# Performance work log

Measured on AMD Instinct MI355X. Metric: run time of the kernel, lower is better.

## Reference

```python
import jax, jax.numpy as jnp
import numpy as np

NB, NR = 100000, 200000            # bridge / road node counts
E_BR, E_RB, E_BB = 1000000, 1000000, 500000  # edges per relation
H = 32                             # hidden_channels


def _sage(h_src, h_dst, src, dst, n_dst, Wl, bl, Wr):
    # PyG SAGEConv: lin_l(mean_{j in N(i)} x_j) + lin_r(x_i); lin_r has no bias
    msg = jnp.take(h_src, src, axis=0)                      # [E, H] gather
    s = jax.ops.segment_sum(msg, dst, num_segments=n_dst)   # [n_dst, H] scatter-add
    cnt = jax.ops.segment_sum(jnp.ones((dst.shape[0],), h_src.dtype), dst, num_segments=n_dst)
    mean = s / jnp.maximum(cnt, 1.0)[:, None]                # mean aggregation
    return mean @ Wl + bl + h_dst @ Wr


def setup_inputs():
    key = jax.random.key(0)
    ks = jax.random.split(key, 24)
    n = lambda i, shape, s=0.1: jax.random.normal(ks[i], shape, jnp.float32) * s
    return {
        "x_bridge": n(0, (NB, 16), 1.0),
        "x_road": n(1, (NR, 8), 1.0),
        "src_br": jax.random.randint(ks[2], (E_BR,), 0, NB),
        "dst_br": jax.random.randint(ks[3], (E_BR,), 0, NR),
        "src_rb": jax.random.randint(ks[4], (E_RB,), 0, NR),
        "dst_rb": jax.random.randint(ks[5], (E_RB,), 0, NB),
        "src_bb": jax.random.randint(ks[6], (E_BB,), 0, NB),
        "dst_bb": jax.random.randint(ks[7], (E_BB,), 0, NB),
        "W_enc_b": n(8, (16, H)), "b_enc_b": n(9, (H,)),
        "W_enc_r": n(10, (8, H)), "b_enc_r": n(11, (H,)),
        "Wl_br": n(12, (H, H)), "bl_br": n(13, (H,)), "Wr_br": n(14, (H, H)),
        "Wl_rb": n(15, (H, H)), "bl_rb": n(16, (H,)), "Wr_rb": n(17, (H, H)),
        "Wl_bb": n(18, (H, H)), "bl_bb": n(19, (H,)), "Wr_bb": n(20, (H, H)),
        "Wo": n(21, (H, 1)), "bo": n(22, (1,)),
    }


def reference(x_bridge, x_road, src_br, dst_br, src_rb, dst_rb, src_bb, dst_bb,
              W_enc_b, b_enc_b, W_enc_r, b_enc_r,
              Wl_br, bl_br, Wr_br, Wl_rb, bl_rb, Wr_rb, Wl_bb, bl_bb, Wr_bb,
              Wo, bo):
    # per-node-type encoder + relu
    h_b = jax.nn.relu(x_bridge @ W_enc_b + b_enc_b)          # [NB, H]
    h_r = jax.nn.relu(x_road @ W_enc_r + b_enc_r)            # [NR, H]
    # HeteroConv(aggr='sum'): 'bridge' receives road->bridge and bridge->bridge.
    # (bridge->road output is dead code w.r.t. the returned bridge head; XLA DCEs it.)
    out_b = (_sage(h_r, h_b, src_rb, dst_rb, NB, Wl_rb, bl_rb, Wr_rb)
             + _sage(h_b, h_b, src_bb, dst_bb, NB, Wl_bb, bl_bb, Wr_bb))
    # relu then output Linear on 'bridge'
    return jax.nn.relu(out_b) @ Wo + bo                       # [NB, 1]
```

## Files before the change

### kernel.cpp

```cpp
#include <hip/hip_runtime.h>
#include <hip/hip_fp16.h>

#define H 32
#define TPB 256
#define EPT 16
#define SLOTS 128
#define CAP 2048
#define SUPB 2048
#define CAP1 22528
#define K2 4
#define NSUPMAX 128

__global__ void __launch_bounds__(TPB) prep_kernel(
        const float* __restrict__ x_b, const float* __restrict__ x_r,
        const float* __restrict__ W_b, const float* __restrict__ b_b,
        const float* __restrict__ W_r, const float* __restrict__ b_r,
        __half* __restrict__ h_b16, __half* __restrict__ h_r16,
        int NB, int NR, int encBlocks,
        const int* __restrict__ src_rb, const int* __restrict__ dst_rb,
        const int* __restrict__ src_bb, const int* __restrict__ dst_bb,
        int* __restrict__ gcur1, int* __restrict__ bins1,
        int E_RB, int E_BB, int NSUP) {
    int t = threadIdx.x;

    if (blockIdx.x < encBlocks) {
        __shared__ float sWb[16][H];
        __shared__ float sWr8[8][H];
        __shared__ float sbb[H];
        __shared__ float sbr[H];
        for (int i = t; i < 16 * H; i += TPB) ((float*)sWb)[i] = W_b[i];
        for (int i = t; i < 8 * H; i += TPB) ((float*)sWr8)[i] = W_r[i];
        if (t < H) { sbb[t] = b_b[t]; sbr[t] = b_r[t]; }
        __syncthreads();

        long long node = (long long)blockIdx.x * TPB + t;
        if (node < NB) {
            const float4* px = (const float4*)(x_b + node * 16);
            float acc[H];
            #pragma unroll
            for (int j = 0; j < H; ++j) acc[j] = sbb[j];
            #pragma unroll
            for (int c = 0; c < 4; ++c) {
                float4 q = px[c];
                float xs[4] = {q.x, q.y, q.z, q.w};
                #pragma unroll
                for (int u = 0; u < 4; ++u) {
                    int k = c * 4 + u;
                    #pragma unroll
                    for (int j = 0; j < H; ++j)
                        acc[j] = fmaf(xs[u], sWb[k][j], acc[j]);
                }
            }
            __half2 o[H / 2];
            #pragma unroll
            for (int j2 = 0; j2 < H / 2; ++j2)
                o[j2] = __floats2half2_rn(fmaxf(acc[2 * j2], 0.0f), fmaxf(acc[2 * j2 + 1], 0.0f));
            float4* dst = (float4*)(h_b16 + node * H);
            const float4* src = (const float4*)o;
            dst[0] = src[0]; dst[1] = src[1]; dst[2] = src[2]; dst[3] = src[3];
        } else if (node < (long long)NB + NR) {
            long long m = node - NB;
            const float4* px = (const float4*)(x_r + m * 8);
            float acc[H];
            #pragma unroll
            for (int j = 0; j < H; ++j) acc[j] = sbr[j];
            #pragma unroll
            for (int c = 0; c < 2; ++c) {
                float4 q = px[c];
                float xs[4] = {q.x, q.y, q.z, q.w};
                #pragma unroll
                for (int u = 0; u < 4; ++u) {
                    int k = c * 4 + u;
                    #pragma unroll
                    for (int j = 0; j < H; ++j)
                        acc[j] = fmaf(xs[u], sWr8[k][j], acc[j]);
                }
            }
            __half2 o[H / 2];
            #pragma unroll
            for (int j2 = 0; j2 < H / 2; ++j2)
                o[j2] = __floats2half2_rn(fmaxf(acc[2 * j2], 0.0f), fmaxf(acc[2 * j2 + 1], 0.0f));
            float4* dst = (float4*)(h_r16 + m * H);
            const float4* src = (const float4*)o;
            dst[0] = src[0]; dst[1] = src[1]; dst[2] = src[2]; dst[3] = src[3];
        }
    } else {
        __shared__ int lcnt[NSUPMAX];
        __shared__ int wbase[NSUPMAX];
        if (t < NSUPMAX) { lcnt[t] = 0; }
        __syncthreads();

        long long e0 = (long long)(blockIdx.x - encBlocks) * (TPB * EPT);
        long long EA = (long long)E_RB + E_BB;
        long long rb4 = (long long)(E_RB >> 2);
        int meta[EPT];

        #pragma unroll
        for (int j = 0; j < EPT / 4; ++j) {
            long long i4 = (e0 >> 2) + (long long)j * TPB + t;
            long long eb = i4 << 2;
            int dd[4];
            if (eb + 3 < (long long)E_RB) {
                int4 dv = ((const int4*)dst_rb)[i4];
                dd[0] = dv.x; dd[1] = dv.y; dd[2] = dv.z; dd[3] = dv.w;
            } else if (eb >= (long long)E_RB && eb + 3 < EA) {
                int4 dv = ((const int4*)dst_bb)[i4 - rb4];
                dd[0] = dv.x + NB; dd[1] = dv.y + NB; dd[2] = dv.z + NB; dd[3] = dv.w + NB;
            } else {
                #pragma unroll
                for (int u = 0; u < 4; ++u) {
                    long long e = eb + u;
                    dd[u] = (e < E_RB) ? dst_rb[e] : (e < EA ? NB + dst_bb[e - E_RB] : -1);
                }
            }
            #pragma unroll
            for (int u = 0; u < 4; ++u) {
                if (dd[u] >= 0) {
                    int sup = dd[u] >> 11;
                    int loc = atomicAdd(&lcnt[sup], 1);
                    meta[j * 4 + u] = (sup << 23) | (loc << 11) | (dd[u] & 2047);
                } else meta[j * 4 + u] = -1;
            }
        }
        __syncthreads();

        if (t < NSUP) {
            int c = lcnt[t];
            wbase[t] = c ? (t * CAP1 + atomicAdd(&gcur1[t * 16], c)) : 0;
        }
        __syncthreads();

        #pragma unroll
        for (int j = 0; j < EPT / 4; ++j) {
            long long i4 = (e0 >> 2) + (long long)j * TPB + t;
            long long eb = i4 << 2;
            int ss[4];
            if (eb + 3 < (long long)E_RB) {
                int4 sv = ((const int4*)src_rb)[i4];
                ss[0] = sv.x; ss[1] = sv.y; ss[2] = sv.z; ss[3] = sv.w;
            } else if (eb >= (long long)E_RB && eb + 3 < EA) {
                int4 sv = ((const int4*)src_bb)[i4 - rb4];
                ss[0] = sv.x; ss[1] = sv.y; ss[2] = sv.z; ss[3] = sv.w;
            } else {
                #pragma unroll
                for (int u = 0; u < 4; ++u) {
                    long long e = eb + u;
                    ss[u] = (e < E_RB) ? src_rb[e] : (e < EA ? (int)src_bb[e - E_RB] : 0);
                }
            }
            #pragma unroll
            for (int u = 0; u < 4; ++u) {
                int m = meta[j * 4 + u];
                if (m >= 0) {
                    int sup = (unsigned)m >> 23;
                    int loc = (m >> 11) & 0xFFF;
                    int gslot = wbase[sup] + loc;
                    if (gslot < (sup + 1) * CAP1)
                        bins1[gslot] = (ss[u] << 11) | (m & 2047);
                }
            }
        }
    }
}

__global__ void __launch_bounds__(TPB) placeB_kernel(
        const int* __restrict__ bins1, const int* __restrict__ gcur1,
        int* __restrict__ gcur2, int* __restrict__ bins, int NBUCK) {
    __shared__ int lcnt[16];
    __shared__ int wbase[16];
    __shared__ int lcur[16];
    int t = threadIdx.x;
    int sup = blockIdx.x / K2;
    int j   = blockIdx.x % K2;
    int n = gcur1[sup * 16];
    if (n > CAP1) n = CAP1;
    int chunk = (n + K2 - 1) / K2;
    int lo = j * chunk;
    int hi = lo + chunk; if (hi > n) hi = n;

    if (t < 16) lcnt[t] = 0;
    __syncthreads();

    const int* __restrict__ seg = bins1 + (long long)sup * CAP1;
    for (int i = lo + t; i < hi; i += TPB)
        atomicAdd(&lcnt[(seg[i] >> 7) & 15], 1);
    __syncthreads();

    if (t < 16) {
        int c = lcnt[t];
        int fb = sup * 16 + t;
        wbase[t] = (c && fb < NBUCK) ? (fb * CAP + atomicAdd(&gcur2[fb * 16], c)) : 0;
        lcur[t] = 0;
    }
    __syncthreads();

    for (int i = lo + t; i < hi; i += TPB) {
        int p = seg[i];
        int f = (p >> 7) & 15;
        int loc = atomicAdd(&lcur[f], 1);
        int fb = sup * 16 + f;
        int gslot = wbase[f] + loc;
        if (gslot < (fb + 1) * CAP)
            bins[gslot] = ((p >> 11) << 7) | (p & 127);
    }
}

__global__ void __launch_bounds__(TPB) buildgather_kernel(
        const __half* __restrict__ h_r16, const __half* __restrict__ h_b16,
        const int* __restrict__ bins, const int* __restrict__ gcur2,
        __half* __restrict__ mean16, int NB, int N2) {
    __shared__ int rawbuf[CAP];
    __shared__ int srcbuf[CAP];
    __shared__ int lcnt[SLOTS];
    __shared__ int lbase[SLOTS];
    __shared__ int lcur[SLOTS];
    __shared__ int tmp[SLOTS];
    int t = threadIdx.x;
    int b = blockIdx.x;
    int start = b * CAP;
    int n = gcur2[b * 16];
    if (n > CAP) n = CAP;

    if (t < SLOTS) lcnt[t] = 0;
    __syncthreads();

    {
        int n4 = n >> 2;
        const int4* bins4 = (const int4*)(bins + start);
        for (int i = t; i < n4; i += TPB) {
            int4 p = bins4[i];
            ((int4*)rawbuf)[i] = p;
            atomicAdd(&lcnt[p.x & 127], 1);
            atomicAdd(&lcnt[p.y & 127], 1);
            atomicAdd(&lcnt[p.z & 127], 1);
            atomicAdd(&lcnt[p.w & 127], 1);
        }
        for (int i = (n4 << 2) + t; i < n; i += TPB) {
            int packed = bins[start + i];
            rawbuf[i] = packed;
            atomicAdd(&lcnt[packed & 127], 1);
        }
    }
    __syncthreads();

    if (t < SLOTS) tmp[t] = lcnt[t];
    __syncthreads();
    for (int off = 1; off < SLOTS; off <<= 1) {
        int x = (t >= off && t < SLOTS) ? tmp[t - off] : 0;
        __syncthreads();
        if (t < SLOTS) tmp[t] += x;
        __syncthreads();
    }
    if (t < SLOTS) { lbase[t] = tmp[t] - lcnt[t]; lcur[t] = tmp[t] - lcnt[t]; }
    __syncthreads();

    for (int i = t; i < n; i += TPB) {
        int packed = rawbuf[i];
        int slot = atomicAdd(&lcur[packed & 127], 1);
        srcbuf[slot] = packed >> 7;
    }
    __syncthreads();

    int lane = t & 15, g = t >> 4;
    long long base_slot = (long long)b << 7;
    for (int sl = g; sl < SLOTS; sl += (TPB / 16)) {
        long long gd = base_slot + sl;
        if (gd >= N2) break;
        const __half* __restrict__ hs = (gd < NB) ? h_r16 : h_b16;
        int off = lbase[sl];
        int cnt = lcnt[sl];
        float ax = 0.0f, ay = 0.0f;
        int k = 0;
        for (; k + 8 <= cnt; k += 8) {
            int s[8];
            #pragma unroll
            for (int jj = 0; jj < 8; ++jj) s[jj] = srcbuf[off + k + jj];
            float2 f[8];
            #pragma unroll
            for (int jj = 0; jj < 8; ++jj)
                f[jj] = __half22float2(*(const __half2*)(hs + (long long)s[jj] * H + 2 * lane));
            #pragma unroll
            for (int jj = 0; jj < 8; ++jj) { ax += f[jj].x; ay += f[jj].y; }
        }
        if (k + 4 <= cnt) {
            int s[4];
            #pragma unroll
            for (int jj = 0; jj < 4; ++jj) s[jj] = srcbuf[off + k + jj];
            float2 f[4];
            #pragma unroll
            for (int jj = 0; jj < 4; ++jj)
                f[jj] = __half22float2(*(const __half2*)(hs + (long long)s[jj] * H + 2 * lane));
            #pragma unroll
            for (int jj = 0; jj < 4; ++jj) { ax += f[jj].x; ay += f[jj].y; }
            k += 4;
        }
        for (; k < cnt; ++k) {
            int s = srcbuf[off + k];
            float2 f = __half22float2(*(const __half2*)(hs + (long long)s * H + 2 * lane));
            ax += f.x; ay += f.y;
        }
        float inv = 1.0f / fmaxf((float)cnt, 1.0f);
        *(__half2*)(mean16 + gd * H + 2 * lane) = __floats2half2_rn(ax * inv, ay * inv);
    }
}

__global__ void __launch_bounds__(TPB) head_kernel(
        const __half* __restrict__ h_b16,
        const __half* __restrict__ mean16,
        const float* __restrict__ Wl_rb,
        const float* __restrict__ bl_rb,
        const float* __restrict__ Wl_bb,
        const float* __restrict__ bl_bb,
        const float* __restrict__ Wr_rb,
        const float* __restrict__ Wr_bb,
        const float* __restrict__ Wo,
        const float* __restrict__ bo,
        float* __restrict__ y, int N) {
    __shared__ float sWl_rb[H][H];
    __shared__ float sWl_bb[H][H];
    __shared__ float sWr[H][H];
    __shared__ float sbl[H];
    __shared__ float sWo[H];
    __shared__ float sbo;

    int t = threadIdx.x;
    for (int i = t; i < H * H; i += blockDim.x) {
        ((float*)sWl_rb)[i] = Wl_rb[i];
        ((float*)sWl_bb)[i] = Wl_bb[i];
        ((float*)sWr)[i]    = Wr_rb[i] + Wr_bb[i];
    }
    if (t < H) {
        sbl[t] = bl_rb[t] + bl_bb[t];
        sWo[t] = Wo[t];
    }
    if (t == 0) sbo = bo[0];
    __syncthreads();

    int node = blockIdx.x * TPB + t;
    if (node >= N) return;

    const float4* pr = (const float4*)(mean16 + (long long)node * H);
    const float4* pb = (const float4*)(mean16 + ((long long)N + node) * H);
    const float4* ph = (const float4*)(h_b16 + (long long)node * H);

    float acc[H];
    #pragma unroll
    for (int j = 0; j < H; ++j) acc[j] = sbl[j];

    #pragma unroll
    for (int c = 0; c < 4; ++c) {
        float4 qr = pr[c];
        float4 qb = pb[c];
        float4 qh = ph[c];
        const __half2* hr = (const __half2*)&qr;
        const __half2* hb = (const __half2*)&qb;
        const __half2* hh = (const __half2*)&qh;
        #pragma unroll
        for (int u = 0; u < 4; ++u) {
            float2 fr = __half22float2(hr[u]);
            float2 fb = __half22float2(hb[u]);
            float2 fh = __half22float2(hh[u]);
            int k0 = c * 8 + u * 2;
            #pragma unroll
            for (int j = 0; j < H; ++j) {
                acc[j] = fmaf(fr.x, sWl_rb[k0][j], acc[j]);
                acc[j] = fmaf(fb.x, sWl_bb[k0][j], acc[j]);
                acc[j] = fmaf(fh.x, sWr[k0][j], acc[j]);
                acc[j] = fmaf(fr.y, sWl_rb[k0 + 1][j], acc[j]);
                acc[j] = fmaf(fb.y, sWl_bb[k0 + 1][j], acc[j]);
                acc[j] = fmaf(fh.y, sWr[k0 + 1][j], acc[j]);
            }
        }
    }

    float out = 0.0f;
    #pragma unroll
    for (int j = 0; j < H; ++j)
        out = fmaf(fmaxf(acc[j], 0.0f), sWo[j], out);
    y[node] = out + sbo;
}

extern "C" void kernel_launch(void* const* d_in, const int* in_sizes, int n_in,
                              void* d_out, int out_size, void* d_ws, size_t ws_size,
                              hipStream_t stream) {
    const float* x_bridge = (const float*)d_in[0];
    const float* x_road   = (const float*)d_in[1];
    const int* src_rb = (const int*)d_in[4];
    const int* dst_rb = (const int*)d_in[5];
    const int* src_bb = (const int*)d_in[6];
    const int* dst_bb = (const int*)d_in[7];
    const float* W_enc_b = (const float*)d_in[8];
    const float* b_enc_b = (const float*)d_in[9];
    const float* W_enc_r = (const float*)d_in[10];
    const float* b_enc_r = (const float*)d_in[11];
    const float* Wl_rb = (const float*)d_in[15];
    const float* bl_rb = (const float*)d_in[16];
    const float* Wr_rb = (const float*)d_in[17];
    const float* Wl_bb = (const float*)d_in[18];
    const float* bl_bb = (const float*)d_in[19];
    const float* Wr_bb = (const float*)d_in[20];
    const float* Wo = (const float*)d_in[21];
    const float* bo = (const float*)d_in[22];
    float* y = (float*)d_out;

    const int NB = in_sizes[0] / 16;
    const int NR = in_sizes[1] / 8;
    const int E_RB = in_sizes[4];
    const int E_BB = in_sizes[6];
    const int N2 = 2 * NB;
    const long long E_ALL = (long long)E_RB + E_BB;
    const int NBUCK = (N2 + SLOTS - 1) / SLOTS;
    const int NSUP  = (N2 + SUPB - 1) / SUPB;

    char* wp = (char*)d_ws;
    __half* h_r16  = (__half*)wp; wp += (size_t)NR * H * sizeof(__half);
    __half* h_b16  = (__half*)wp; wp += (size_t)NB * H * sizeof(__half);
    __half* mean16 = (__half*)wp; wp += (size_t)N2 * H * sizeof(__half);
    int* bins1 = (int*)wp;       wp += (size_t)NSUP * CAP1 * sizeof(int);
    int* bins  = (int*)wp;       wp += (size_t)NBUCK * CAP * sizeof(int);
    int* gcur1 = (int*)wp;       wp += (size_t)NSUP * 16 * sizeof(int);
    int* gcur2 = (int*)wp;       wp += (size_t)NBUCK * 16 * sizeof(int);

    hipMemsetAsync(gcur1, 0, (size_t)(NSUP + NBUCK) * 16 * sizeof(int), stream);

    long long nodes = (long long)NB + NR;
    int encBlocks = (int)((nodes + TPB - 1) / TPB);
    int placeBlocks = (int)((E_ALL + (TPB * EPT) - 1) / (TPB * EPT));
    prep_kernel<<<encBlocks + placeBlocks, TPB, 0, stream>>>(
        x_bridge, x_road, W_enc_b, b_enc_b, W_enc_r, b_enc_r,
        h_b16, h_r16, NB, NR, encBlocks,
        src_rb, dst_rb, src_bb, dst_bb, gcur1, bins1, E_RB, E_BB, NSUP);

    placeB_kernel<<<NSUP * K2, TPB, 0, stream>>>(bins1, gcur1, gcur2, bins, NBUCK);

    buildgather_kernel<<<NBUCK, TPB, 0, stream>>>(h_r16, h_b16, bins, gcur2,
                                                  mean16, NB, N2);

    head_kernel<<<(NB + TPB - 1) / TPB, TPB, 0, stream>>>(h_b16, mean16,
                                                  Wl_rb, bl_rb, Wl_bb, bl_bb,
                                                  Wr_rb, Wr_bb, Wo, bo, y, NB);
}
```

Before: 94.86 us.

## Interleave rb/bb destination slots and fuse head into gather kernel

Destination indices are remapped so each bridge node's road->bridge and bridge->bridge slots sit next to each other (2*d and 2*d+1). Each 128-slot bucket then holds all aggregates for 64 bridge nodes, so the head linear/relu/output computation is appended to the gather kernel and the separate head kernel launch is removed. This saves a launch and lets the head read mean values the same block just wrote, which should still be in cache. In exchange, only 64 threads per block run the head, reading weights from global memory instead of shared memory, which may raise per-block latency.

```diff
diff --git a/kernel.cpp b/kernel.cpp
--- a/kernel.cpp
+++ b/kernel.cpp
@@ -102,15 +102,16 @@
             int dd[4];
             if (eb + 3 < (long long)E_RB) {
                 int4 dv = ((const int4*)dst_rb)[i4];
-                dd[0] = dv.x; dd[1] = dv.y; dd[2] = dv.z; dd[3] = dv.w;
+                dd[0] = 2 * dv.x; dd[1] = 2 * dv.y; dd[2] = 2 * dv.z; dd[3] = 2 * dv.w;
             } else if (eb >= (long long)E_RB && eb + 3 < EA) {
                 int4 dv = ((const int4*)dst_bb)[i4 - rb4];
-                dd[0] = dv.x + NB; dd[1] = dv.y + NB; dd[2] = dv.z + NB; dd[3] = dv.w + NB;
+                dd[0] = 2 * dv.x + 1; dd[1] = 2 * dv.y + 1; dd[2] = 2 * dv.z + 1; dd[3] = 2 * dv.w + 1;
             } else {
                 #pragma unroll
                 for (int u = 0; u < 4; ++u) {
                     long long e = eb + u;
-                    dd[u] = (e < E_RB) ? dst_rb[e] : (e < EA ? NB + dst_bb[e - E_RB] : -1);
+                    dd[u] = (e < E_RB) ? 2 * dst_rb[e]
+                                       : (e < EA ? 2 * dst_bb[e - E_RB] + 1 : -1);
                 }
             }
             #pragma unroll
@@ -208,7 +209,12 @@
 __global__ void __launch_bounds__(TPB) buildgather_kernel(
         const __half* __restrict__ h_r16, const __half* __restrict__ h_b16,
         const int* __restrict__ bins, const int* __restrict__ gcur2,
-        __half* __restrict__ mean16, int NB, int N2) {
+        __half* __restrict__ mean16, int NB, int N2,
+        const float* __restrict__ Wl_rb, const float* __restrict__ bl_rb,
+        const float* __restrict__ Wl_bb, const float* __restrict__ bl_bb,
+        const float* __restrict__ Wr_rb, const float* __restrict__ Wr_bb,
+        const float* __restrict__ Wo, const float* __restrict__ bo,
+        float* __restrict__ y) {
     __shared__ int rawbuf[CAP];
     __shared__ int srcbuf[CAP];
     __shared__ int lcnt[SLOTS];
@@ -266,7 +272,7 @@
     for (int sl = g; sl < SLOTS; sl += (TPB / 16)) {
         long long gd = base_slot + sl;
         if (gd >= N2) break;
-        const __half* __restrict__ hs = (gd < NB) ? h_r16 : h_b16;
+        const __half* __restrict__ hs = (gd & 1) ? h_b16 : h_r16;
         int off = lbase[sl];
         int cnt = lcnt[sl];
         float ax = 0.0f, ay = 0.0f;
@@ -302,82 +308,53 @@
         float inv = 1.0f / fmaxf((float)cnt, 1.0f);
         *(__half2*)(mean16 + gd * H + 2 * lane) = __floats2half2_rn(ax * inv, ay * inv);
     }
-}
-
-__global__ void __launch_bounds__(TPB) head_kernel(
-        const __half* __restrict__ h_b16,
-        const __half* __restrict__ mean16,
-        const float* __restrict__ Wl_rb,
-        const float* __restrict__ bl_rb,
-        const float* __restrict__ Wl_bb,
-        const float* __restrict__ bl_bb,
-        const float* __restrict__ Wr_rb,
-        const float* __restrict__ Wr_bb,
-        const float* __restrict__ Wo,
-        const float* __restrict__ bo,
-        float* __restrict__ y, int N) {
-    __shared__ float sWl_rb[H][H];
-    __shared__ float sWl_bb[H][H];
-    __shared__ float sWr[H][H];
-    __shared__ float sbl[H];
-    __shared__ float sWo[H];
-    __shared__ float sbo;
-
-    int t = threadIdx.x;
-    for (int i = t; i < H * H; i += blockDim.x) {
-        ((float*)sWl_rb)[i] = Wl_rb[i];
-        ((float*)sWl_bb)[i] = Wl_bb[i];
-        ((float*)sWr)[i]    = Wr_rb[i] + Wr_bb[i];
-    }
-    if (t < H) {
-        sbl[t] = bl_rb[t] + bl_bb[t];
-        sWo[t] = Wo[t];
-    }
-    if (t == 0) sbo = bo[0];
-    __syncthreads();
-
-    int node = blockIdx.x * TPB + t;
-    if (node >= N) return;
-
-    const float4* pr = (const float4*)(mean16 + (long long)node * H);
-    const float4* pb = (const float4*)(mean16 + ((long long)N + node) * H);
-    const float4* ph = (const float4*)(h_b16 + (long long)node * H);
-
-    float acc[H];
-    #pragma unroll
-    for (int j = 0; j < H; ++j) acc[j] = sbl[j];
-
-    #pragma unroll
-    for (int c = 0; c < 4; ++c) {
-        float4 qr = pr[c];
-        float4 qb = pb[c];
-        float4 qh = ph[c];
-        const __half2* hr = (const __half2*)&qr;
-        const __half2* hb = (const __half2*)&qb;
-        const __half2* hh = (const __half2*)&qh;
-        #pragma unroll
-        for (int u = 0; u < 4; ++u) {
-            float2 fr = __half22float2(hr[u]);
-            float2 fb = __half22float2(hb[u]);
-            float2 fh = __half22float2(hh[u]);
-            int k0 = c * 8 + u * 2;
-            #pragma unroll
-            for (int j = 0; j < H; ++j) {
-                acc[j] = fmaf(fr.x, sWl_rb[k0][j], acc[j]);
-                acc[j] = fmaf(fb.x, sWl_bb[k0][j], acc[j]);
-                acc[j] = fmaf(fh.x, sWr[k0][j], acc[j]);
-                acc[j] = fmaf(fr.y, sWl_rb[k0 + 1][j], acc[j]);
-                acc[j] = fmaf(fb.y, sWl_bb[k0 + 1][j], acc[j]);
-                acc[j] = fmaf(fh.y, sWr[k0 + 1][j], acc[j]);
-            }
-        }
-    }
-
-    float out = 0.0f;
-    #pragma unroll
-    for (int j = 0; j < H; ++j)
-        out = fmaf(fmaxf(acc[j], 0.0f), sWo[j], out);
-    y[node] = out + sbo;
+
+    __threadfence_block();
+    __syncthreads();
+
+    if (t < 64) {
+        int node = b * 64 + t;
+        if (node < NB) {
+            const float4* pm = (const float4*)(mean16 + (long long)(2 * node) * H);
+            const float4* ph = (const float4*)(h_b16 + (long long)node * H);
+
+            float acc[H];
+            #pragma unroll
+            for (int j = 0; j < H; ++j) acc[j] = bl_rb[j] + bl_bb[j];
+
+            #pragma unroll
+            for (int c = 0; c < 4; ++c) {
+                float4 qr = pm[c];
+                float4 qb = pm[4 + c];
+                float4 qh = ph[c];
+                const __half2* hr = (const __half2*)&qr;
+                const __half2* hb = (const __half2*)&qb;
+                const __half2* hh = (const __half2*)&qh;
+                #pragma unroll
+                for (int u = 0; u < 4; ++u) {
+                    float2 fr = __half22float2(hr[u]);
+                    float2 fb = __half22float2(hb[u]);
+                    float2 fh = __half22float2(hh[u]);
+                    int k0 = c * 8 + u * 2;
+                    #pragma unroll
+                    for (int j = 0; j < H; ++j) {
+                        acc[j] = fmaf(fr.x, Wl_rb[k0 * H + j], acc[j]);
+                        acc[j] = fmaf(fb.x, Wl_bb[k0 * H + j], acc[j]);
+                        acc[j] = fmaf(fh.x, Wr_rb[k0 * H + j] + Wr_bb[k0 * H + j], acc[j]);
+                        acc[j] = fmaf(fr.y, Wl_rb[(k0 + 1) * H + j], acc[j]);
+                        acc[j] = fmaf(fb.y, Wl_bb[(k0 + 1) * H + j], acc[j]);
+                        acc[j] = fmaf(fh.y, Wr_rb[(k0 + 1) * H + j] + Wr_bb[(k0 + 1) * H + j], acc[j]);
+                    }
+                }
+            }
+
+            float out = 0.0f;
+            #pragma unroll
+            for (int j = 0; j < H; ++j)
+                out = fmaf(fmaxf(acc[j], 0.0f), Wo[j], out);
+            y[node] = out + bo[0];
+        }
+    }
 }
 
 extern "C" void kernel_launch(void* const* d_in, const int* in_sizes, int n_in,
@@ -434,9 +411,7 @@
     placeB_kernel<<<NSUP * K2, TPB, 0, stream>>>(bins1, gcur1, gcur2, bins, NBUCK);
 
     buildgather_kernel<<<NBUCK, TPB, 0, stream>>>(h_r16, h_b16, bins, gcur2,
-                                                  mean16, NB, N2);
-
-    head_kernel<<<(NB + TPB - 1) / TPB, TPB, 0, stream>>>(h_b16, mean16,
+                                                  mean16, NB, N2,
                                                   Wl_rb, bl_rb, Wl_bb, bl_bb,
-                                                  Wr_rb, Wr_bb, Wo, bo, y, NB);
+                                                  Wr_rb, Wr_bb, Wo, bo, y);
 }
```

Result: slower. 106.5 us (+12.2%).
